# Performance work log

Hardware: AMD Instinct MI355X
Metric: run time of the kernel (lower is better)

Reference implementation:

```python
import jax, jax.numpy as jnp
import numpy as np

B, S, D, H, L, EXP = 2, 2048, 512, 8, 2, 4
WORD_VOCAB, TAG_VOCAB = 50000, 1000
LN_EPS = 1e-3  # keras LayerNormalization default


def _sinusoidal(seq_len, dim):
    pos = jnp.arange(seq_len, dtype=jnp.float32)[:, None]          # [S,1]
    i = jnp.arange(dim // 2, dtype=jnp.float32)[None, :]           # [1,D/2]
    ang = pos / (10000.0 ** (2.0 * i / dim))                       # [S,D/2]
    return jnp.concatenate([jnp.sin(ang), jnp.cos(ang)], axis=-1)  # [S,D]


def _layer_norm(x, scale, bias):
    mu = jnp.mean(x, axis=-1, keepdims=True)
    var = jnp.mean(jnp.square(x - mu), axis=-1, keepdims=True)
    return (x - mu) * jax.lax.rsqrt(var + LN_EPS) * scale + bias


def _attention(x, mask, Wq, Wk, Wv, Wo):
    b, s, d = x.shape
    dh = d // H
    def split(t):
        return t.reshape(b, s, H, dh).transpose(0, 2, 1, 3)  # [B,H,S,dh]
    q, k, v = split(x @ Wq), split(x @ Wk), split(x @ Wv)
    scores = jnp.einsum('bhqd,bhkd->bhqk', q, k) / jnp.sqrt(jnp.float32(dh))
    scores = jnp.where(mask[:, None, None, :], scores, jnp.float32(-1e9))
    probs = jax.nn.softmax(scores, axis=-1)
    out = jnp.einsum('bhqk,bhkd->bhqd', probs, v)
    out = out.transpose(0, 2, 1, 3).reshape(b, s, d)
    return out @ Wo


def setup_inputs() -> dict:
    key = jax.random.key(0)
    ks = jax.random.split(key, 20)
    sc = 0.02
    inp = {
        'ids': jax.random.randint(ks[0], (B, S), 0, WORD_VOCAB),
        'mask': jnp.ones((B, S), dtype=bool),
        'emb': jax.random.normal(ks[1], (WORD_VOCAB, D), jnp.float32) * sc,
        'ln1_s': jnp.ones((L, D), jnp.float32),
        'ln1_b': jnp.zeros((L, D), jnp.float32),
        'Wq': jax.random.normal(ks[2], (L, D, D), jnp.float32) * sc,
        'Wk': jax.random.normal(ks[3], (L, D, D), jnp.float32) * sc,
        'Wv': jax.random.normal(ks[4], (L, D, D), jnp.float32) * sc,
        'Wo': jax.random.normal(ks[5], (L, D, D), jnp.float32) * sc,
        'ln2_s': jnp.ones((L, D), jnp.float32),
        'ln2_b': jnp.zeros((L, D), jnp.float32),
        'W1': jax.random.normal(ks[6], (L, D, D * EXP), jnp.float32) * sc,
        'b1': jnp.zeros((L, D * EXP), jnp.float32),
        'W2': jax.random.normal(ks[7], (L, D * EXP, D), jnp.float32) * sc,
        'b2': jnp.zeros((L, D), jnp.float32),
        'Wout': jax.random.normal(ks[8], (D, TAG_VOCAB), jnp.float32) * sc,
        'bout': jnp.zeros((TAG_VOCAB,), jnp.float32),
    }
    return inp


def reference(ids, mask, emb, ln1_s, ln1_b, Wq, Wk, Wv, Wo, ln2_s, ln2_b, W1, b1, W2, b2, Wout, bout):
    x = emb[ids]                       # [B,S,D]
    h = x + _sinusoidal(S, D)[None]    # add positional embedding
    for l in range(L):
        a = _layer_norm(h, ln1_s[l], ln1_b[l])
        h = h + _attention(a, mask, Wq[l], Wk[l], Wv[l], Wo[l])
        f = _layer_norm(h, ln2_s[l], ln2_b[l])
        f = jax.nn.relu(f @ W1[l] + b1[l]) @ W2[l] + b2[l]
        h = h + f
    return jax.nn.softmax(h @ Wout + bout, axis=-1)  # [B,S,TAG_VOCAB]
```

## Files before the change

### kernel.cpp

```cpp
#include <hip/hip_runtime.h>
#include <hip/hip_bf16.h>
#include <math.h>

#define S_LEN   2048
#define D_MODEL 512
#define N_ROWS  4096
#define D_FF    2048
#define N_TAGS  1000
#define LNEPS   1e-3f
#define ATP     72
#define PSTR    80

using bf16x8_t = __attribute__((ext_vector_type(8))) __bf16;
using f32x4_t  = __attribute__((ext_vector_type(4))) float;

__device__ __forceinline__ f32x4_t mfma16(bf16x8_t a, bf16x8_t b, f32x4_t c) {
    return __builtin_amdgcn_mfma_f32_16x16x32_bf16(a, b, c, 0, 0, 0);
}
__device__ __forceinline__ bf16x8_t ldsf(const __hip_bfloat16* p) {
    return *(const bf16x8_t*)p;
}
typedef const __attribute__((address_space(1))) void gvoid_t;
typedef __attribute__((address_space(3))) void lvoid_t;
__device__ __forceinline__ void gload16(const void* g, void* l) {
    __builtin_amdgcn_global_load_lds((gvoid_t*)g, (lvoid_t*)l, 16, 0, 0);
}

__global__ __launch_bounds__(256) void k_embed_ln(
    const int* __restrict__ ids, const float* __restrict__ emb,
    const double* __restrict__ freqd,
    const float* __restrict__ gamma, const float* __restrict__ beta,
    float* __restrict__ h, __hip_bfloat16* __restrict__ y)
{
    int t = threadIdx.x, wave = t >> 6, lane = t & 63;
    int row = blockIdx.x * 4 + wave;
    int s = row & (S_LEN - 1);
    int c = lane * 8;
    const float* er = emb + (size_t)ids[row] * D_MODEL + c;
    float vv[8];
    #pragma unroll
    for (int j = 0; j < 8; ++j) {
        int d = c + j;
        double ang = freqd[d & 255] * (double)s;
        double kr  = rint(ang * 0.15915494309189535);
        double r   = fma(-kr, 6.283185307179586, ang);
        float rf = (float)r;
        float pe = (d < 256) ? sinf(rf) : cosf(rf);
        vv[j] = er[j] + pe;
    }
    float* hr = h + (size_t)row * D_MODEL + c;
    *(float4*)hr       = make_float4(vv[0], vv[1], vv[2], vv[3]);
    *(float4*)(hr + 4) = make_float4(vv[4], vv[5], vv[6], vv[7]);

    float ssum = 0.f;
    #pragma unroll
    for (int j = 0; j < 8; ++j) ssum += vv[j];
    #pragma unroll
    for (int off = 1; off < 64; off <<= 1) ssum += __shfl_xor(ssum, off);
    float mean = ssum * (1.0f / D_MODEL);
    float var = 0.f;
    #pragma unroll
    for (int j = 0; j < 8; ++j) { vv[j] -= mean; var += vv[j] * vv[j]; }
    #pragma unroll
    for (int off = 1; off < 64; off <<= 1) var += __shfl_xor(var, off);
    float rstd = 1.0f / sqrtf(var * (1.0f / D_MODEL) + LNEPS);
    float4 g0 = *(const float4*)(gamma + c);
    float4 g1 = *(const float4*)(gamma + c + 4);
    float4 b0 = *(const float4*)(beta + c);
    float4 b1 = *(const float4*)(beta + c + 4);
    float gg[8] = {g0.x, g0.y, g0.z, g0.w, g1.x, g1.y, g1.z, g1.w};
    float bb[8] = {b0.x, b0.y, b0.z, b0.w, b1.x, b1.y, b1.z, b1.w};
    union { uint4 u; __hip_bfloat16 b[8]; } pk;
    #pragma unroll
    for (int j = 0; j < 8; ++j) pk.b[j] = __float2bfloat16(vv[j] * rstd * gg[j] + bb[j]);
    *(uint4*)(y + (size_t)row * D_MODEL + c) = pk.u;
}

__global__ __launch_bounds__(256) void k_layernorm(
    const float* __restrict__ x, const float* __restrict__ gamma,
    const float* __restrict__ beta, __hip_bfloat16* __restrict__ y)
{
    int t = threadIdx.x, wave = t >> 6, lane = t & 63;
    int row = blockIdx.x * 4 + wave;
    const float* xr = x + (size_t)row * D_MODEL;
    int c = lane * 8;
    float4 v0 = *(const float4*)(xr + c);
    float4 v1 = *(const float4*)(xr + c + 4);
    float vv[8] = {v0.x, v0.y, v0.z, v0.w, v1.x, v1.y, v1.z, v1.w};
    float s = 0.f;
    #pragma unroll
    for (int i = 0; i < 8; ++i) s += vv[i];
    #pragma unroll
    for (int off = 1; off < 64; off <<= 1) s += __shfl_xor(s, off);
    float mean = s * (1.0f / D_MODEL);
    float var = 0.f;
    #pragma unroll
    for (int i = 0; i < 8; ++i) { vv[i] -= mean; var += vv[i] * vv[i]; }
    #pragma unroll
    for (int off = 1; off < 64; off <<= 1) var += __shfl_xor(var, off);
    float rstd = 1.0f / sqrtf(var * (1.0f / D_MODEL) + LNEPS);
    float4 g0 = *(const float4*)(gamma + c);
    float4 g1 = *(const float4*)(gamma + c + 4);
    float4 b0 = *(const float4*)(beta + c);
    float4 b1 = *(const float4*)(beta + c + 4);
    float gg[8] = {g0.x, g0.y, g0.z, g0.w, g1.x, g1.y, g1.z, g1.w};
    float bb[8] = {b0.x, b0.y, b0.z, b0.w, b1.x, b1.y, b1.z, b1.w};
    union { uint4 u; __hip_bfloat16 b[8]; } pk;
    #pragma unroll
    for (int i = 0; i < 8; ++i) pk.b[i] = __float2bfloat16(vv[i] * rstd * gg[i] + bb[i]);
    *(uint4*)(y + (size_t)row * D_MODEL + c) = pk.u;
}

__global__ __launch_bounds__(256) void k_wtrans_all(
    const float* __restrict__ Wq, const float* __restrict__ Wk,
    const float* __restrict__ Wv, const float* __restrict__ Wo,
    const float* __restrict__ W1, const float* __restrict__ W2,
    const float* __restrict__ Wout,
    __hip_bfloat16* __restrict__ Wqkv_t, __hip_bfloat16* __restrict__ Wo_t,
    __hip_bfloat16* __restrict__ W1_t,   __hip_bfloat16* __restrict__ W2_t,
    __hip_bfloat16* __restrict__ Wout_t, double* __restrict__ freqd)
{
    int idx = blockIdx.x;
    if (idx == 0 && threadIdx.x < 256)
        freqd[threadIdx.x] = exp(-9.210340371976184 * ((double)threadIdx.x * (1.0 / 256.0)));
    const float* src; __hip_bfloat16* dst;
    int K, N, ntile, ktile;
    if (idx < 384) {
        int l = idx / 192, r = idx % 192;
        int mat = r / 64, rr = r % 64;
        ntile = rr / 8; ktile = rr % 8;
        src = (mat == 0 ? Wq : mat == 1 ? Wk : Wv) + (size_t)l * 512 * 512;
        dst = Wqkv_t + (size_t)l * 1536 * 512 + (size_t)mat * 512 * 512;
        K = 512; N = 512;
    } else if (idx < 512) {
        int i = idx - 384; int l = i / 64, rr = i % 64;
        ntile = rr / 8; ktile = rr % 8;
        src = Wo + (size_t)l * 512 * 512; dst = Wo_t + (size_t)l * 512 * 512;
        K = 512; N = 512;
    } else if (idx < 1024) {
        int i = idx - 512; int l = i / 256, rr = i % 256;
        ntile = rr / 8; ktile = rr % 8;
        src = W1 + (size_t)l * 512 * 2048; dst = W1_t + (size_t)l * 2048 * 512;
        K = 512; N = 2048;
    } else if (idx < 1536) {
        int i = idx - 1024; int l = i / 256, rr = i % 256;
        ntile = rr / 32; ktile = rr % 32;
        src = W2 + (size_t)l * 2048 * 512; dst = W2_t + (size_t)l * 512 * 2048;
        K = 2048; N = 512;
    } else {
        int i = idx - 1536;
        ntile = i / 8; ktile = i % 8;
        src = Wout; dst = Wout_t; K = 512; N = 1000;
    }
    __shared__ float tile[64][65];
    int k0 = ktile * 64, n0 = ntile * 64;
    int t = threadIdx.x, c = t & 63, r4 = t >> 6;
    for (int rr = r4; rr < 64; rr += 4) {
        int n = n0 + c;
        tile[rr][c] = (n < N) ? src[(size_t)(k0 + rr) * N + n] : 0.0f;
    }
    __syncthreads();
    for (int rr = r4; rr < 64; rr += 4)
        dst[(size_t)(n0 + rr) * K + k0 + c] = __float2bfloat16(tile[c][rr]);
}

__global__ __launch_bounds__(256) void k_gemm_sk(
    const __hip_bfloat16* __restrict__ A,
    const __hip_bfloat16* __restrict__ Bt,
    float* __restrict__ Cf, __hip_bfloat16* __restrict__ Cb,
    __hip_bfloat16* __restrict__ Cb2,
    const float* __restrict__ bias, const float* __restrict__ res,
    __hip_bfloat16* __restrict__ vtb,
    int K, int Nc, int relu)
{
    __shared__ __align__(16) char smem[36864];
    float* sc = (float*)smem;

    int t = threadIdx.x, wave = t >> 6, lane = t & 63;
    int quad = lane >> 4, l16 = lane & 15;
    int m0 = blockIdx.y << 6, n0 = blockIdx.x << 6;

    const char* Ag = (const char*)(A + (size_t)(m0 + (t >> 2)) * K) + (t & 3) * 16;
    const char* Bg = (const char*)(Bt + (size_t)(n0 + (t >> 2)) * K) + (t & 3) * 16;
    char* Asl = (char*)smem + t * 16;
    char* Bsl = (char*)smem + 16384 + t * 16;

    f32x4_t zero = {0.f, 0.f, 0.f, 0.f};
    f32x4_t acc[4][4];
    #pragma unroll
    for (int i = 0; i < 4; ++i)
        #pragma unroll
        for (int j = 0; j < 4; ++j) acc[i][j] = zero;

    const __hip_bfloat16* Asub = (__hip_bfloat16*)smem + wave * 2048;
    const __hip_bfloat16* Bsub = (__hip_bfloat16*)(smem + 16384) + wave * 2048;

    for (int k0 = 0; k0 < K; k0 += 128) {
        __syncthreads();
        #pragma unroll
        for (int w = 0; w < 4; ++w) {
            gload16(Ag + (size_t)k0 * 2 + w * 64, Asl + w * 4096);
            gload16(Bg + (size_t)k0 * 2 + w * 64, Bsl + w * 4096);
        }
        __syncthreads();
        bf16x8_t af[4], bfv[4];
        #pragma unroll
        for (int i = 0; i < 4; ++i)
            af[i] = ldsf(&Asub[(i * 16 + l16) * 32 + quad * 8]);
        #pragma unroll
        for (int j = 0; j < 4; ++j)
            bfv[j] = ldsf(&Bsub[(j * 16 + l16) * 32 + quad * 8]);
        #pragma unroll
        for (int i = 0; i < 4; ++i)
            #pragma unroll
            for (int j = 0; j < 4; ++j)
                acc[i][j] = mfma16(af[i], bfv[j], acc[i][j]);
    }

    __syncthreads();
    if (wave == 1 || wave == 3) {
        float* d = sc + (wave >> 1) * 4096;
        #pragma unroll
        for (int i = 0; i < 4; ++i)
            #pragma unroll
            for (int j = 0; j < 4; ++j)
                *(f32x4_t*)(d + (i * 4 + j) * 256 + lane * 4) = acc[i][j];
    }
    __syncthreads();
    if (wave == 0 || wave == 2) {
        const float* s = sc + (wave >> 1) * 4096;
        #pragma unroll
        for (int i = 0; i < 4; ++i)
            #pragma unroll
            for (int j = 0; j < 4; ++j)
                acc[i][j] += *(const f32x4_t*)(s + (i * 4 + j) * 256 + lane * 4);
    }
    __syncthreads();
    if (wave == 0) {
        #pragma unroll
        for (int i = 2; i < 4; ++i)
            #pragma unroll
            for (int j = 0; j < 4; ++j)
                *(f32x4_t*)(sc + ((i - 2) * 4 + j) * 256 + lane * 4) = acc[i][j];
    }
    if (wave == 2) {
        #pragma unroll
        for (int i = 0; i < 2; ++i)
            #pragma unroll
            for (int j = 0; j < 4; ++j)
                *(f32x4_t*)(sc + 2048 + (i * 4 + j) * 256 + lane * 4) = acc[i][j];
    }
    __syncthreads();
    float* rm = (float*)(smem + 16384);
    if (wave == 0) {
        #pragma unroll
        for (int i = 0; i < 2; ++i)
            #pragma unroll
            for (int j = 0; j < 4; ++j) {
                acc[i][j] += *(const f32x4_t*)(sc + 2048 + (i * 4 + j) * 256 + lane * 4);
                #pragma unroll
                for (int r = 0; r < 4; ++r)
                    rm[(i * 16 + quad * 4 + r) * 68 + j * 16 + l16] = acc[i][j][r];
            }
    }
    if (wave == 2) {
        #pragma unroll
        for (int i = 2; i < 4; ++i)
            #pragma unroll
            for (int j = 0; j < 4; ++j) {
                acc[i][j] += *(const f32x4_t*)(sc + ((i - 2) * 4 + j) * 256 + lane * 4);
                #pragma unroll
                for (int r = 0; r < 4; ++r)
                    rm[(i * 16 + quad * 4 + r) * 68 + j * 16 + l16] = acc[i][j][r];
            }
    }
    __syncthreads();

    if (vtb && n0 >= 1024) {
        int d = t >> 2, sb = (t & 3) << 4;
        union { uint4 u[2]; __hip_bfloat16 b[16]; } pk;
        #pragma unroll
        for (int k = 0; k < 16; ++k)
            pk.b[k] = __float2bfloat16(rm[(sb + k) * 68 + d]);
        int head = (n0 - 1024) >> 6;
        int bb = m0 >> 11, s0 = m0 & (S_LEN - 1);
        __hip_bfloat16* dstp = vtb + ((size_t)((bb << 3) + head) * 64 + d) * S_LEN + s0 + sb;
        *(uint4*)dstp = pk.u[0];
        *(uint4*)(dstp + 8) = pk.u[1];
        return;
    }

    {
        int row = t >> 2, cb = (t & 3) << 4;
        const float* rmp = rm + row * 68 + cb;
        int gr = m0 + row, gc = n0 + cb;
        float v[16];
        #pragma unroll
        for (int x = 0; x < 16; x += 4) {
            f32x4_t q = *(const f32x4_t*)(rmp + x);
            v[x] = q[0]; v[x + 1] = q[1]; v[x + 2] = q[2]; v[x + 3] = q[3];
        }
        if (gc + 15 < Nc) {
            if (bias) {
                #pragma unroll
                for (int x = 0; x < 16; x += 4) {
                    float4 bq = *(const float4*)(bias + gc + x);
                    v[x] += bq.x; v[x + 1] += bq.y; v[x + 2] += bq.z; v[x + 3] += bq.w;
                }
            }
            if (relu) {
                #pragma unroll
                for (int x = 0; x < 16; ++x) v[x] = fmaxf(v[x], 0.0f);
            }
            size_t base = (size_t)gr * Nc + gc;
            if (res) {
                #pragma unroll
                for (int x = 0; x < 16; x += 4) {
                    float4 rq = *(const float4*)(res + base + x);
                    v[x] += rq.x; v[x + 1] += rq.y; v[x + 2] += rq.z; v[x + 3] += rq.w;
                }
            }
            if (Cf) {
                #pragma unroll
                for (int x = 0; x < 16; x += 4)
                    *(float4*)(Cf + base + x) = make_float4(v[x], v[x + 1], v[x + 2], v[x + 3]);
            }
            if (Cb || Cb2) {
                union { uint4 u[2]; __hip_bfloat16 b[16]; } pk;
                #pragma unroll
                for (int x = 0; x < 16; ++x) pk.b[x] = __float2bfloat16(v[x]);
                if (Cb) {
                    *(uint4*)(Cb + base)     = pk.u[0];
                    *(uint4*)(Cb + base + 8) = pk.u[1];
                }
                if (Cb2) {
                    *(uint4*)(Cb2 + base)     = pk.u[0];
                    *(uint4*)(Cb2 + base + 8) = pk.u[1];
                }
            }
        } else if (gc < Nc) {
            for (int x = 0; x < 16 && gc + x < Nc; ++x) {
                float val = v[x];
                if (bias) val += bias[gc + x];
                if (relu) val = fmaxf(val, 0.0f);
                size_t idx = (size_t)gr * Nc + gc + x;
                if (res) val += res[idx];
                if (Cf) Cf[idx] = val;
                if (Cb) Cb[idx] = __float2bfloat16(val);
                if (Cb2) Cb2[idx] = __float2bfloat16(val);
            }
        }
    }
}

__global__ __launch_bounds__(256) void k_attn_mfma(
    const __hip_bfloat16* __restrict__ qkv,
    const __hip_bfloat16* __restrict__ vtb,
    __hip_bfloat16* __restrict__ o)
{
    __shared__ __align__(16) __hip_bfloat16 Qs[64 * ATP];
    __shared__ __align__(16) __hip_bfloat16 Ks[64 * ATP];
    __shared__ __align__(16) __hip_bfloat16 Vs[64 * ATP];
    __shared__ __align__(16) __hip_bfloat16 Ps[64 * PSTR];

    int t = threadIdx.x, wave = t >> 6, lane = t & 63;
    int quad = lane >> 4, l16 = lane & 15;
    int bh = blockIdx.y, bb = bh >> 3, hh = bh & 7;
    int q0 = blockIdx.x << 6;
    size_t rb = (size_t)bb * S_LEN;
    int qoff = hh * 64, koff = 512 + hh * 64;
    const __hip_bfloat16* vhead = vtb + (size_t)bh * 64 * S_LEN;

    #pragma unroll
    for (int u = 0; u < 2; ++u) {
        int slot = t + u * 256, row = slot >> 3, oct = slot & 7;
        *(uint4*)&Qs[row * ATP + oct * 8] =
            *(const uint4*)&qkv[(rb + q0 + row) * 1536 + qoff + oct * 8];
    }
    float m_i = -1e30f, l_i = 0.0f;
    f32x4_t zero = {0.f, 0.f, 0.f, 0.f};
    f32x4_t oacc[4];
    #pragma unroll
    for (int nt = 0; nt < 4; ++nt) oacc[nt] = zero;

    const int prow = (wave * 16 + l16) * PSTR;

    for (int kt = 0; kt < S_LEN; kt += 64) {
        __syncthreads();
        #pragma unroll
        for (int u = 0; u < 2; ++u) {
            int slot = t + u * 256, row = slot >> 3, oct = slot & 7;
            *(uint4*)&Ks[row * ATP + oct * 8] =
                *(const uint4*)&qkv[(rb + kt + row) * 1536 + koff + oct * 8];
            *(uint4*)&Vs[row * ATP + oct * 8] =
                *(const uint4*)&vhead[(size_t)row * S_LEN + kt + oct * 8];
        }
        __syncthreads();

        bf16x8_t qf0 = ldsf(&Qs[(wave * 16 + l16) * ATP + quad * 8]);
        bf16x8_t qf1 = ldsf(&Qs[(wave * 16 + l16) * ATP + 32 + quad * 8]);
        f32x4_t s[4];
        #pragma unroll
        for (int jt = 0; jt < 4; ++jt) {
            f32x4_t z = mfma16(ldsf(&Ks[(jt * 16 + l16) * ATP + quad * 8]),      qf0, zero);
            z        = mfma16(ldsf(&Ks[(jt * 16 + l16) * ATP + 32 + quad * 8]), qf1, z);
            s[jt] = z * 0.125f;
        }
        float mx = -1e30f;
        #pragma unroll
        for (int jt = 0; jt < 4; ++jt)
            #pragma unroll
            for (int r = 0; r < 4; ++r) mx = fmaxf(mx, s[jt][r]);
        mx = fmaxf(mx, __shfl_xor(mx, 16));
        mx = fmaxf(mx, __shfl_xor(mx, 32));
        float mn = fmaxf(m_i, mx);
        float alpha = __expf(m_i - mn);
        m_i = mn;
        float ps = 0.f;
        #pragma unroll
        for (int jt = 0; jt < 4; ++jt)
            #pragma unroll
            for (int r = 0; r < 4; ++r) {
                float p = __expf(s[jt][r] - mn);
                s[jt][r] = p;
                ps += p;
            }
        ps += __shfl_xor(ps, 16);
        ps += __shfl_xor(ps, 32);
        l_i = l_i * alpha + ps;

        #pragma unroll
        for (int jt = 0; jt < 4; ++jt) {
            union { ushort4 u; __hip_bfloat16 b[4]; } pk;
            #pragma unroll
            for (int r = 0; r < 4; ++r) pk.b[r] = __float2bfloat16(s[jt][r]);
            *(ushort4*)&Ps[prow + jt * 16 + quad * 4] = pk.u;
        }
        float aro[4];
        #pragma unroll
        for (int r = 0; r < 4; ++r) aro[r] = __shfl(alpha, quad * 4 + r);
        #pragma unroll
        for (int nt = 0; nt < 4; ++nt)
            #pragma unroll
            for (int r = 0; r < 4; ++r) oacc[nt][r] *= aro[r];
        bf16x8_t pf0 = ldsf(&Ps[prow + quad * 8]);
        bf16x8_t pf1 = ldsf(&Ps[prow + 32 + quad * 8]);
        #pragma unroll
        for (int nt = 0; nt < 4; ++nt) {
            f32x4_t ov = oacc[nt];
            ov = mfma16(pf0, ldsf(&Vs[(nt * 16 + l16) * ATP + quad * 8]), ov);
            ov = mfma16(pf1, ldsf(&Vs[(nt * 16 + l16) * ATP + 32 + quad * 8]), ov);
            oacc[nt] = ov;
        }
    }
    float linv[4];
    #pragma unroll
    for (int r = 0; r < 4; ++r) linv[r] = 1.0f / __shfl(l_i, quad * 4 + r);
    #pragma unroll
    for (int nt = 0; nt < 4; ++nt)
        #pragma unroll
        for (int r = 0; r < 4; ++r)
            o[(rb + q0 + wave * 16 + quad * 4 + r) * 512 + hh * 64 + nt * 16 + l16] =
                __float2bfloat16(oacc[nt][r] * linv[r]);
}

__global__ __launch_bounds__(256) void k_softmax_rows(float* x)
{
    int t = threadIdx.x, wave = t >> 6, lane = t & 63;
    int row = blockIdx.x * 4 + wave;
    float* xr = x + (size_t)row * N_TAGS;
    float z[16];
    float mx = -INFINITY;
    #pragma unroll
    for (int i = 0; i < 16; ++i) {
        int c = lane + i * 64;
        z[i] = (c < N_TAGS) ? xr[c] : -INFINITY;
        mx = fmaxf(mx, z[i]);
    }
    #pragma unroll
    for (int off = 1; off < 64; off <<= 1) mx = fmaxf(mx, __shfl_xor(mx, off));
    float s = 0.f;
    #pragma unroll
    for (int i = 0; i < 16; ++i) {
        int c = lane + i * 64;
        if (c < N_TAGS) { z[i] = expf(z[i] - mx); s += z[i]; }
    }
    #pragma unroll
    for (int off = 1; off < 64; off <<= 1) s += __shfl_xor(s, off);
    float inv = 1.0f / s;
    #pragma unroll
    for (int i = 0; i < 16; ++i) {
        int c = lane + i * 64;
        if (c < N_TAGS) xr[c] = z[i] * inv;
    }
}

extern "C" void kernel_launch(void* const* d_in, const int* in_sizes, int n_in,
                              void* d_out, int out_size, void* d_ws, size_t ws_size,
                              hipStream_t stream)
{
    (void)in_sizes; (void)n_in; (void)out_size; (void)ws_size;
    const int*   ids  = (const int*)d_in[0];
    const float* emb  = (const float*)d_in[2];
    const float* ln1s = (const float*)d_in[3];
    const float* ln1b = (const float*)d_in[4];
    const float* Wq   = (const float*)d_in[5];
    const float* Wk   = (const float*)d_in[6];
    const float* Wv   = (const float*)d_in[7];
    const float* Wo   = (const float*)d_in[8];
    const float* ln2s = (const float*)d_in[9];
    const float* ln2b = (const float*)d_in[10];
    const float* W1   = (const float*)d_in[11];
    const float* b1   = (const float*)d_in[12];
    const float* W2   = (const float*)d_in[13];
    const float* b2   = (const float*)d_in[14];
    const float* Wout = (const float*)d_in[15];
    const float* bout = (const float*)d_in[16];
    float* out = (float*)d_out;

    char* w = (char*)d_ws;
    auto alloc = [&](size_t bytes) { char* p = w; w += (bytes + 255) & ~(size_t)255; return p; };
    float*          h      = (float*)         alloc((size_t)N_ROWS * 512 * 4);
    double*         freqd  = (double*)        alloc(256 * 8);
    __hip_bfloat16* alnb   = (__hip_bfloat16*)alloc((size_t)N_ROWS * 512 * 2);
    __hip_bfloat16* qkvb   = (__hip_bfloat16*)alloc((size_t)N_ROWS * 1536 * 2);
    __hip_bfloat16* vtb    = (__hip_bfloat16*)alloc((size_t)1024 * S_LEN * 2);
    __hip_bfloat16* attnb  = (__hip_bfloat16*)alloc((size_t)N_ROWS * 512 * 2);
    __hip_bfloat16* midb   = (__hip_bfloat16*)alloc((size_t)N_ROWS * 2048 * 2);
    __hip_bfloat16* hbf    = (__hip_bfloat16*)alloc((size_t)N_ROWS * 512 * 2);
    __hip_bfloat16* Wqkv_t = (__hip_bfloat16*)alloc((size_t)2 * 1536 * 512 * 2);
    __hip_bfloat16* Wo_t   = (__hip_bfloat16*)alloc((size_t)2 * 512 * 512 * 2);
    __hip_bfloat16* W1_t   = (__hip_bfloat16*)alloc((size_t)2 * 2048 * 512 * 2);
    __hip_bfloat16* W2_t   = (__hip_bfloat16*)alloc((size_t)2 * 512 * 2048 * 2);
    __hip_bfloat16* Wout_t = (__hip_bfloat16*)alloc((size_t)1024 * 512 * 2);

    k_wtrans_all<<<1664, 256, 0, stream>>>(Wq, Wk, Wv, Wo, W1, W2, Wout,
                                           Wqkv_t, Wo_t, W1_t, W2_t, Wout_t, freqd);
    k_embed_ln<<<N_ROWS / 4, 256, 0, stream>>>(ids, emb, freqd, ln1s, ln1b, h, alnb);

    for (int l = 0; l < 2; ++l) {
        if (l > 0)
            k_layernorm<<<N_ROWS / 4, 256, 0, stream>>>(h, ln1s + l*512, ln1b + l*512, alnb);
        k_gemm_sk<<<dim3(24, 64), 256, 0, stream>>>(alnb, Wqkv_t + (size_t)l*1536*512,
                                                    nullptr, qkvb, nullptr, nullptr, nullptr,
                                                    vtb, 512, 1536, 0);
        k_attn_mfma<<<dim3(32, 16), 256, 0, stream>>>(qkvb, vtb, attnb);
        k_gemm_sk<<<dim3(8, 64), 256, 0, stream>>>(attnb, Wo_t + (size_t)l*512*512,
                                                   h, nullptr, nullptr, nullptr, h,
                                                   nullptr, 512, 512, 0);
        k_layernorm<<<N_ROWS / 4, 256, 0, stream>>>(h, ln2s + l*512, ln2b + l*512, alnb);
        k_gemm_sk<<<dim3(32, 64), 256, 0, stream>>>(alnb, W1_t + (size_t)l*2048*512,
                                                    nullptr, midb, nullptr, b1 + l*2048, nullptr,
                                                    nullptr, 512, 2048, 1);
        k_gemm_sk<<<dim3(8, 64), 256, 0, stream>>>(midb, W2_t + (size_t)l*512*2048,
                                                   h, nullptr, (l == 1) ? hbf : nullptr,
                                                   b2 + l*512, h, nullptr, 2048, 512, 0);
    }

    k_gemm_sk<<<dim3(16, 64), 256, 0, stream>>>(hbf, Wout_t, out, nullptr, nullptr,
                                                bout, nullptr, nullptr, 512, 1000, 0);
    k_softmax_rows<<<N_ROWS / 4, 256, 0, stream>>>(out);
}
```

Before: 508.0 us.

## Add dedicated 128x64 bf16 GEMM for QKV/FFN1 and shrink attention query tiles

Adds a new two-wave GEMM kernel with 128x64 tiles and direct register-to-global epilogue, used for the QKV projection (including the transposed V write) and the first FFN matmul, replacing the split-K style kernel there. The attention kernel now processes 32 query rows per 128-thread block, doubling the number of blocks for better occupancy. The intent is to cut the LDS round-trip epilogue and the split-K reduction overhead, and to spread attention across more CUs, at the cost of less K/V reuse per block and scattered 2-byte stores in the GEMM epilogue.

```diff
diff --git a/kernel.cpp b/kernel.cpp
--- a/kernel.cpp
+++ b/kernel.cpp
@@ -9,7 +9,7 @@
 #define N_TAGS  1000
 #define LNEPS   1e-3f
 #define ATP     72
-#define PSTR    80
+#define PSTR    72
 
 using bf16x8_t = __attribute__((ext_vector_type(8))) __bf16;
 using f32x4_t  = __attribute__((ext_vector_type(4))) float;
@@ -164,13 +164,97 @@
         dst[(size_t)(n0 + rr) * K + k0 + c] = __float2bfloat16(tile[c][rr]);
 }
 
+__global__ __launch_bounds__(128) void k_gemm_bt(
+    const __hip_bfloat16* __restrict__ A,
+    const __hip_bfloat16* __restrict__ Bt,
+    __hip_bfloat16* __restrict__ Cb,
+    const float* __restrict__ bias, int relu, int K, int Nc,
+    __hip_bfloat16* __restrict__ vtb)
+{
+    __shared__ __align__(16) __hip_bfloat16 As[128 * 32];
+    __shared__ __align__(16) __hip_bfloat16 Bs[64 * 32];
+    int t = threadIdx.x, wave = t >> 6, lane = t & 63;
+    int quad = lane >> 4, l16 = lane & 15;
+    int m0 = blockIdx.y << 7, n0 = blockIdx.x << 6;
+
+    const char* Ag = (const char*)(A + (size_t)(m0 + (t >> 2)) * K) + (t & 3) * 16;
+    const char* Bg = (const char*)(Bt + (size_t)(n0 + (t >> 2)) * K) + (t & 3) * 16;
+    char* Asl = (char*)As + t * 16;
+    char* Bsl = (char*)Bs + t * 16;
+    size_t ask = (size_t)32 * K * 2;
+
+    f32x4_t zero = {0.f, 0.f, 0.f, 0.f};
+    f32x4_t acc[4][4];
+    #pragma unroll
+    for (int i = 0; i < 4; ++i)
+        #pragma unroll
+        for (int j = 0; j < 4; ++j) acc[i][j] = zero;
+
+    for (int k0 = 0; k0 < K; k0 += 32) {
+        __syncthreads();
+        size_t kb = (size_t)k0 * 2;
+        #pragma unroll
+        for (int u = 0; u < 4; ++u)
+            gload16(Ag + kb + u * ask, Asl + u * 2048);
+        #pragma unroll
+        for (int u = 0; u < 2; ++u)
+            gload16(Bg + kb + u * ask, Bsl + u * 2048);
+        __syncthreads();
+        bf16x8_t af[4], bfv[4];
+        #pragma unroll
+        for (int i = 0; i < 4; ++i)
+            af[i] = ldsf(&As[(wave * 64 + i * 16 + l16) * 32 + quad * 8]);
+        #pragma unroll
+        for (int j = 0; j < 4; ++j)
+            bfv[j] = ldsf(&Bs[(j * 16 + l16) * 32 + quad * 8]);
+        #pragma unroll
+        for (int i = 0; i < 4; ++i)
+            #pragma unroll
+            for (int j = 0; j < 4; ++j)
+                acc[i][j] = mfma16(af[i], bfv[j], acc[i][j]);
+    }
+
+    if (vtb && n0 >= 1024) {
+        int head = (n0 - 1024) >> 6;
+        int bb = m0 >> 11, s0 = (m0 & (S_LEN - 1)) + wave * 64;
+        #pragma unroll
+        for (int j = 0; j < 4; ++j) {
+            int d = j * 16 + l16;
+            __hip_bfloat16* dp = vtb + ((size_t)((bb << 3) + head) * 64 + d) * S_LEN + s0;
+            #pragma unroll
+            for (int i = 0; i < 4; ++i) {
+                union { ushort4 u; __hip_bfloat16 b[4]; } pk;
+                #pragma unroll
+                for (int r = 0; r < 4; ++r) pk.b[r] = __float2bfloat16(acc[i][j][r]);
+                *(ushort4*)(dp + i * 16 + quad * 4) = pk.u;
+            }
+        }
+        return;
+    }
+
+    #pragma unroll
+    for (int j = 0; j < 4; ++j) {
+        int col = n0 + j * 16 + l16;
+        float bv = bias ? bias[col] : 0.0f;
+        #pragma unroll
+        for (int i = 0; i < 4; ++i) {
+            int rowb = m0 + wave * 64 + i * 16 + quad * 4;
+            #pragma unroll
+            for (int r = 0; r < 4; ++r) {
+                float v = acc[i][j][r] + bv;
+                if (relu) v = fmaxf(v, 0.0f);
+                Cb[(size_t)(rowb + r) * Nc + col] = __float2bfloat16(v);
+            }
+        }
+    }
+}
+
 __global__ __launch_bounds__(256) void k_gemm_sk(
     const __hip_bfloat16* __restrict__ A,
     const __hip_bfloat16* __restrict__ Bt,
     float* __restrict__ Cf, __hip_bfloat16* __restrict__ Cb,
     __hip_bfloat16* __restrict__ Cb2,
     const float* __restrict__ bias, const float* __restrict__ res,
-    __hip_bfloat16* __restrict__ vtb,
     int K, int Nc, int relu)
 {
     __shared__ __align__(16) char smem[36864];
@@ -275,20 +359,6 @@
             }
     }
     __syncthreads();
-
-    if (vtb && n0 >= 1024) {
-        int d = t >> 2, sb = (t & 3) << 4;
-        union { uint4 u[2]; __hip_bfloat16 b[16]; } pk;
-        #pragma unroll
-        for (int k = 0; k < 16; ++k)
-            pk.b[k] = __float2bfloat16(rm[(sb + k) * 68 + d]);
-        int head = (n0 - 1024) >> 6;
-        int bb = m0 >> 11, s0 = m0 & (S_LEN - 1);
-        __hip_bfloat16* dstp = vtb + ((size_t)((bb << 3) + head) * 64 + d) * S_LEN + s0 + sb;
-        *(uint4*)dstp = pk.u[0];
-        *(uint4*)(dstp + 8) = pk.u[1];
-        return;
-    }
 
     {
         int row = t >> 2, cb = (t & 3) << 4;
@@ -353,27 +423,27 @@
     }
 }
 
-__global__ __launch_bounds__(256) void k_attn_mfma(
+__global__ __launch_bounds__(128) void k_attn_mfma(
     const __hip_bfloat16* __restrict__ qkv,
     const __hip_bfloat16* __restrict__ vtb,
     __hip_bfloat16* __restrict__ o)
 {
-    __shared__ __align__(16) __hip_bfloat16 Qs[64 * ATP];
+    __shared__ __align__(16) __hip_bfloat16 Qs[32 * ATP];
     __shared__ __align__(16) __hip_bfloat16 Ks[64 * ATP];
     __shared__ __align__(16) __hip_bfloat16 Vs[64 * ATP];
-    __shared__ __align__(16) __hip_bfloat16 Ps[64 * PSTR];
+    __shared__ __align__(16) __hip_bfloat16 Ps[32 * PSTR];
 
     int t = threadIdx.x, wave = t >> 6, lane = t & 63;
     int quad = lane >> 4, l16 = lane & 15;
     int bh = blockIdx.y, bb = bh >> 3, hh = bh & 7;
-    int q0 = blockIdx.x << 6;
+    int q0 = blockIdx.x << 5;
     size_t rb = (size_t)bb * S_LEN;
     int qoff = hh * 64, koff = 512 + hh * 64;
     const __hip_bfloat16* vhead = vtb + (size_t)bh * 64 * S_LEN;
 
     #pragma unroll
     for (int u = 0; u < 2; ++u) {
-        int slot = t + u * 256, row = slot >> 3, oct = slot & 7;
+        int slot = t + u * 128, row = slot >> 3, oct = slot & 7;
         *(uint4*)&Qs[row * ATP + oct * 8] =
             *(const uint4*)&qkv[(rb + q0 + row) * 1536 + qoff + oct * 8];
     }
@@ -388,8 +458,8 @@
     for (int kt = 0; kt < S_LEN; kt += 64) {
         __syncthreads();
         #pragma unroll
-        for (int u = 0; u < 2; ++u) {
-            int slot = t + u * 256, row = slot >> 3, oct = slot & 7;
+        for (int u = 0; u < 4; ++u) {
+            int slot = t + u * 128, row = slot >> 3, oct = slot & 7;
             *(uint4*)&Ks[row * ATP + oct * 8] =
                 *(const uint4*)&qkv[(rb + kt + row) * 1536 + koff + oct * 8];
             *(uint4*)&Vs[row * ATP + oct * 8] =
@@ -541,23 +611,21 @@
     for (int l = 0; l < 2; ++l) {
         if (l > 0)
             k_layernorm<<<N_ROWS / 4, 256, 0, stream>>>(h, ln1s + l*512, ln1b + l*512, alnb);
-        k_gemm_sk<<<dim3(24, 64), 256, 0, stream>>>(alnb, Wqkv_t + (size_t)l*1536*512,
-                                                    nullptr, qkvb, nullptr, nullptr, nullptr,
-                                                    vtb, 512, 1536, 0);
-        k_attn_mfma<<<dim3(32, 16), 256, 0, stream>>>(qkvb, vtb, attnb);
+        k_gemm_bt<<<dim3(24, 32), 128, 0, stream>>>(alnb, Wqkv_t + (size_t)l*1536*512,
+                                                    qkvb, nullptr, 0, 512, 1536, vtb);
+        k_attn_mfma<<<dim3(64, 16), 128, 0, stream>>>(qkvb, vtb, attnb);
         k_gemm_sk<<<dim3(8, 64), 256, 0, stream>>>(attnb, Wo_t + (size_t)l*512*512,
                                                    h, nullptr, nullptr, nullptr, h,
-                                                   nullptr, 512, 512, 0);
+                                                   512, 512, 0);
         k_layernorm<<<N_ROWS / 4, 256, 0, stream>>>(h, ln2s + l*512, ln2b + l*512, alnb);
-        k_gemm_sk<<<dim3(32, 64), 256, 0, stream>>>(alnb, W1_t + (size_t)l*2048*512,
-                                                    nullptr, midb, nullptr, b1 + l*2048, nullptr,
-                                                    nullptr, 512, 2048, 1);
+        k_gemm_bt<<<dim3(32, 32), 128, 0, stream>>>(alnb, W1_t + (size_t)l*2048*512,
+                                                    midb, b1 + l*2048, 1, 512, 2048, nullptr);
         k_gemm_sk<<<dim3(8, 64), 256, 0, stream>>>(midb, W2_t + (size_t)l*512*2048,
                                                    h, nullptr, (l == 1) ? hbf : nullptr,
-                                                   b2 + l*512, h, nullptr, 2048, 512, 0);
+                                                   b2 + l*512, h, 2048, 512, 0);
     }
 
     k_gemm_sk<<<dim3(16, 64), 256, 0, stream>>>(hbf, Wout_t, out, nullptr, nullptr,
-                                                bout, nullptr, nullptr, 512, 1000, 0);
+                                                bout, nullptr, 512, 1000, 0);
     k_softmax_rows<<<N_ROWS / 4, 256, 0, stream>>>(out);
 }
```

After: 488.6 us. 1.04x faster.
